# Kernel tuning notes

Measured on AMD Instinct MI355X. Metric: run time of the kernel, lower is better.

## Reference

```python
import jax, jax.numpy as jnp
import numpy as np

S, B, D = 4096, 4, 1024
APERTURE = 256
SCALE = 1.0 / np.sqrt(D)
EPS = 1e-6
NEG_INF = -jnp.inf


def _xavier(key, shape, gain=np.sqrt(2.0)):
    fan_in, fan_out = shape[1], shape[0]
    a = gain * np.sqrt(6.0 / (fan_in + fan_out))
    return jax.random.uniform(key, shape, jnp.float32, -a, a)


def setup_inputs() -> dict:
    key = jax.random.key(0)
    ks = jax.random.split(key, 8)
    return {
        "x": jax.random.normal(ks[0], (S, B, D), jnp.float32),
        "Wk": _xavier(ks[1], (D, D)),
        "Wq": _xavier(ks[2], (D, D)),
        "Wv": _xavier(ks[3], (D, D)),
        "Wp": _xavier(ks[4], (D, D)),
        "W1": _xavier(ks[5], (D, D)),
        "b1": jnp.full((D,), 0.1, jnp.float32),
        "W2": _xavier(ks[6], (1, D)),
        "b2": jnp.full((1,), 0.1, jnp.float32),
        "gamma": jnp.ones((D,), jnp.float32),
        "beta": jnp.zeros((D,), jnp.float32),
    }


def _layer_norm(y, gamma, beta):
    m = jnp.mean(y, axis=-1, keepdims=True)
    v = jnp.mean((y - m) ** 2, axis=-1, keepdims=True)
    return (y - m) * jax.lax.rsqrt(v + EPS) * gamma + beta


def reference(x, Wk, Wq, Wv, Wp, W1, b1, W2, b2, gamma, beta):
    # x: (S, B, D) -> (B, S, D)
    xb = jnp.transpose(x, (1, 0, 2))
    K = jnp.einsum('bsd,ed->bse', xb, Wk)
    Q = jnp.einsum('bsd,ed->bse', xb, Wq)
    V = jnp.einsum('bsd,ed->bse', xb, Wv)
    e = jnp.einsum('bqd,bkd->bqk', Q, K) * SCALE  # (B, S, S)
    # ignore_self: -inf on diagonal
    eye = jnp.eye(S, dtype=bool)
    e = jnp.where(eye[None, :, :], NEG_INF, e)
    # aperture mask: torch masks where tril(e,ap)*triu(e,-ap) == 0
    scope = jnp.tril(e, APERTURE) * jnp.triu(e, -APERTURE)
    e = jnp.where(scope == 0, NEG_INF, e)
    alpha = jax.nn.softmax(e, axis=2)  # dropout is identity at eval
    c = jnp.einsum('bqk,bkd->bqd', alpha, V)
    c = jnp.einsum('bqd,ed->bqe', c, Wp)
    y = c + xb
    y = _layer_norm(y, gamma, beta)
    y = jax.nn.relu(jnp.einsum('bsd,ed->bse', y, W1) + b1)
    y = _layer_norm(y, gamma, beta)
    y = jax.nn.sigmoid(jnp.einsum('bsd,ed->bse', y, W2) + b2)  # (B, S, 1)
    return jnp.transpose(y, (1, 0, 2))  # (S, B, 1)
```

## Files before the change

### kernel.cpp

```cpp
#include <hip/hip_runtime.h>
#include <stdint.h>
#include <math.h>

#define S_LEN 4096
#define BATCH 4
#define DIM   1024
#define AP    256
#define NBLK  32
#define BANDC 640
#define SCALE 0.03125f

typedef __attribute__((ext_vector_type(4))) float f32x4;
typedef __attribute__((ext_vector_type(8))) short bf16x8;

__device__ __forceinline__ ushort f2bf(float f) {
  union { float f; uint32_t u; } v; v.f = f;
  uint32_t r = v.u + 0x7FFFu + ((v.u >> 16) & 1u);
  return (ushort)(r >> 16);
}

__device__ __forceinline__ void gload16(const void* g, void* l) {
  __builtin_amdgcn_global_load_lds((const __attribute__((address_space(1))) void*)g,
                                   (__attribute__((address_space(3))) void*)l,
                                   16, 0, 0);
}

__device__ __forceinline__ float block_sum(float v, float* red) {
  #pragma unroll
  for (int o = 32; o > 0; o >>= 1) v += __shfl_xor(v, o, 64);
  const int w = threadIdx.x >> 6;
  if ((threadIdx.x & 63) == 0) red[w] = v;
  __syncthreads();
  v = red[0] + red[1] + red[2] + red[3];
  __syncthreads();
  return v;
}

__device__ __forceinline__ float block_max(float v, float* red) {
  #pragma unroll
  for (int o = 32; o > 0; o >>= 1) v = fmaxf(v, __shfl_xor(v, o, 64));
  const int w = threadIdx.x >> 6;
  if ((threadIdx.x & 63) == 0) red[w] = v;
  __syncthreads();
  v = fmaxf(fmaxf(red[0], red[1]), fmaxf(red[2], red[3]));
  __syncthreads();
  return v;
}

#define STAGE2(dstbase, g0, g1, kcol) \
  gload16((g0) + (kcol), lds + (dstbase) + stOff); \
  gload16((g1) + (kcol), lds + (dstbase) + 4096 + stOff);

#define MFMA_QUAD(arow, bvec) \
  _Pragma("unroll") for (int m = 0; m < 4; ++m) \
  _Pragma("unroll") for (int n = 0; n < 4; ++n) \
    acc[(arow) + m][n] = __builtin_amdgcn_mfma_f32_16x16x32_bf16(a[m], bvec[n], acc[(arow) + m][n], 0, 0, 0);

#define PHASE_TAIL() \
  __builtin_amdgcn_s_barrier(); \
  asm volatile("s_waitcnt lgkmcnt(0)" ::: "memory"); \
  __builtin_amdgcn_s_setprio(1);

#define PHASE_END() \
  __builtin_amdgcn_s_setprio(0); \
  __builtin_amdgcn_s_barrier();

__device__ __forceinline__ void gemm256_core(
    const ushort* __restrict__ Ablk, int lda,
    const ushort* __restrict__ Bblk, int ldb,
    int K, ushort* __restrict__ lds,
    f32x4 acc[8][4])
{
  const int tid  = threadIdx.x;
  const int lane = tid & 63;
  const int wave = tid >> 6;
  const int wr = wave >> 2;
  const int wn = wave & 3;

  const int srow = tid >> 2;
  const int gseg = (tid & 3) ^ ((tid >> 3) & 3);
  const ushort* gA0 = Ablk + (size_t)srow * lda + gseg * 8;
  const ushort* gA1 = Ablk + (size_t)(srow + 128) * lda + gseg * 8;
  const ushort* gB0 = Bblk + (size_t)srow * ldb + gseg * 8;
  const ushort* gB1 = Bblk + (size_t)(srow + 128) * ldb + gseg * 8;
  const int stOff = wave * 512;

  const int l15 = lane & 15;
  const int seg = (lane >> 4) ^ ((lane >> 1) & 3);
  const int raBase = (wr * 128 + l15) * 32 + seg * 8;
  const int rbBase = (wn * 64  + l15) * 32 + seg * 8;

  const int NT = K >> 6;

  STAGE2(0,     gA0, gA1, 0)
  STAGE2(16384, gB0, gB1, 0)
  STAGE2(8192,  gA0, gA1, 32)
  STAGE2(24576, gB0, gB1, 32)
  asm volatile("s_waitcnt vmcnt(4)" ::: "memory");
  __builtin_amdgcn_s_barrier();

  for (int t = 0; t < NT; ++t) {
    const int rb = (t & 1) * 32768;
    const int sb = ((t + 1) & 1) * 32768;
    const int k1 = (t + 1) << 6;
    const bool more = (t + 1 < NT);

    bf16x8 a[4], b0[4], b1[4];

    #pragma unroll
    for (int m = 0; m < 4; ++m) a[m] = *(const bf16x8*)(lds + rb + raBase + m * 512);
    #pragma unroll
    for (int n = 0; n < 4; ++n) b0[n] = *(const bf16x8*)(lds + rb + 16384 + rbBase + n * 512);
    if (more) { STAGE2(sb, gA0, gA1, k1) }
    PHASE_TAIL()
    MFMA_QUAD(0, b0)
    PHASE_END()

    #pragma unroll
    for (int m = 0; m < 4; ++m) a[m] = *(const bf16x8*)(lds + rb + raBase + (m + 4) * 512);
    if (more) {
      STAGE2(sb + 16384, gB0, gB1, k1)
      asm volatile("s_waitcnt vmcnt(4)" ::: "memory");
    } else {
      asm volatile("s_waitcnt vmcnt(0)" ::: "memory");
    }
    PHASE_TAIL()
    MFMA_QUAD(4, b0)
    PHASE_END()

    #pragma unroll
    for (int m = 0; m < 4; ++m) a[m] = *(const bf16x8*)(lds + rb + 8192 + raBase + m * 512);
    #pragma unroll
    for (int n = 0; n < 4; ++n) b1[n] = *(const bf16x8*)(lds + rb + 24576 + rbBase + n * 512);
    if (more) { STAGE2(sb + 8192, gA0, gA1, k1 + 32) }
    PHASE_TAIL()
    MFMA_QUAD(0, b1)
    PHASE_END()

    #pragma unroll
    for (int m = 0; m < 4; ++m) a[m] = *(const bf16x8*)(lds + rb + 8192 + raBase + (m + 4) * 512);
    if (more) {
      STAGE2(sb + 24576, gB0, gB1, k1 + 32)
      asm volatile("s_waitcnt vmcnt(4)" ::: "memory");
    }
    PHASE_TAIL()
    MFMA_QUAD(4, b1)
    PHASE_END()
  }
}

#define ACC256_ZERO(acc) \
  _Pragma("unroll") for (int m_ = 0; m_ < 8; m_++) \
  _Pragma("unroll") for (int n_ = 0; n_ < 4; n_++) \
  _Pragma("unroll") for (int r_ = 0; r_ < 4; r_++) acc[m_][n_][r_] = 0.0f;

__device__ __forceinline__ void epi256_store_bf16(
    f32x4 acc[8][4], ushort* __restrict__ lds,
    ushort* __restrict__ dst, int rowbase, int colb)
{
  __syncthreads();
  const int lane_ = threadIdx.x & 63;
  const int wave_ = threadIdx.x >> 6;
  const int wrb_ = (wave_ >> 2) * 128;
  const int wnb_ = (wave_ & 3) * 64;
  const int rb_ = (lane_ >> 4) << 2;
  const int cb_ = lane_ & 15;
  #pragma unroll
  for (int m = 0; m < 8; m++)
    #pragma unroll
    for (int n = 0; n < 4; n++)
      #pragma unroll
      for (int r = 0; r < 4; r++) {
        const int rl = wrb_ + m * 16 + rb_ + r;
        const int cl = wnb_ + n * 16 + cb_;
        const int cs = cl ^ (((rl >> 2) & 3) << 4);
        lds[rl * 256 + cs] = f2bf(acc[m][n][r]);
      }
  __syncthreads();
  #pragma unroll
  for (int it = 0; it < 16; ++it) {
    const int chunk = it * 512 + threadIdx.x;
    const int rl = chunk >> 5;
    const int c16 = chunk & 31;
    const int csw = (c16 * 16) ^ (((rl >> 2) & 3) << 5);
    bf16x8 v = *(const bf16x8*)((const char*)lds + rl * 512 + csw);
    *(bf16x8*)(dst + (size_t)(rowbase + rl) * DIM + colb + c16 * 8) = v;
  }
}

#define EPI256_BEGIN(acc) { \
  const int lane_ = threadIdx.x & 63; \
  const int wave_ = threadIdx.x >> 6; \
  const int wrb_ = (wave_ >> 2) * 128; \
  const int wnb_ = (wave_ & 3) * 64; \
  const int rb_ = (lane_ >> 4) << 2; \
  const int cb_ = lane_ & 15; \
  _Pragma("unroll") for (int m_ = 0; m_ < 8; m_++) \
  _Pragma("unroll") for (int n_ = 0; n_ < 4; n_++) \
  _Pragma("unroll") for (int r_ = 0; r_ < 4; r_++) { \
    const int rloc = wrb_ + m_ * 16 + rb_ + r_; \
    const int cloc = wnb_ + n_ * 16 + cb_; \
    const float aval = acc[m_][n_][r_];
#define EPI256_END() } }

__device__ __forceinline__ void gemm_core(
    const ushort* __restrict__ Ablk, int lda,
    const ushort* __restrict__ Bblk, int ldb,
    int k_begin, int k_end,
    ushort* __restrict__ lds,
    f32x4 acc[4][4])
{
  const int tid  = threadIdx.x;
  const int lane = tid & 63;
  const int wr = ((tid >> 7) & 1) * 64;
  const int wc = ((tid >> 6) & 1) * 64;
  const int lr = lane & 15;
  const int seg = (lane >> 4) ^ ((lane >> 1) & 3);

  const int srow = tid >> 2;
  const int gseg = (tid & 3) ^ ((tid >> 3) & 3);
  const ushort* gA0 = Ablk + (size_t)srow * lda + gseg * 8;
  const ushort* gA1 = Ablk + (size_t)(srow + 64) * lda + gseg * 8;
  const ushort* gB0 = Bblk + (size_t)srow * ldb + gseg * 8;
  const ushort* gB1 = Bblk + (size_t)(srow + 64) * ldb + gseg * 8;
  const int stA = (tid >> 6) * 512;

  const int NT = (k_end - k_begin) >> 5;

  gload16(gA0 + k_begin, lds + stA);
  gload16(gA1 + k_begin, lds + 2048 + stA);
  gload16(gB0 + k_begin, lds + 4096 + stA);
  gload16(gB1 + k_begin, lds + 6144 + stA);

  for (int t = 0; t < NT; ++t) {
    if (t + 1 < NT) {
      ushort* buf = lds + ((t + 1) & 1) * 8192;
      const int k0 = k_begin + (t + 1) * 32;
      gload16(gA0 + k0, buf + stA);
      gload16(gA1 + k0, buf + 2048 + stA);
      gload16(gB0 + k0, buf + 4096 + stA);
      gload16(gB1 + k0, buf + 6144 + stA);
      asm volatile("s_waitcnt vmcnt(4)" ::: "memory");
    } else {
      asm volatile("s_waitcnt vmcnt(0)" ::: "memory");
    }
    __builtin_amdgcn_s_barrier();

    const ushort* buf = lds + (t & 1) * 8192;
    bf16x8 af[4], bfv[4];
    #pragma unroll
    for (int m = 0; m < 4; m++)
      af[m] = *(const bf16x8*)(buf + (wr + m * 16 + lr) * 32 + seg * 8);
    #pragma unroll
    for (int n = 0; n < 4; n++)
      bfv[n] = *(const bf16x8*)(buf + 4096 + (wc + n * 16 + lr) * 32 + seg * 8);

    __builtin_amdgcn_s_setprio(1);
    #pragma unroll
    for (int m = 0; m < 4; m++)
      #pragma unroll
      for (int n = 0; n < 4; n++)
        acc[m][n] = __builtin_amdgcn_mfma_f32_16x16x32_bf16(af[m], bfv[n], acc[m][n], 0, 0, 0);
    __builtin_amdgcn_s_setprio(0);
    asm volatile("s_waitcnt lgkmcnt(0)" ::: "memory");
  }
}

#define ACC_ZERO(acc) \
  _Pragma("unroll") for (int m_ = 0; m_ < 4; m_++) \
  _Pragma("unroll") for (int n_ = 0; n_ < 4; n_++) \
  _Pragma("unroll") for (int r_ = 0; r_ < 4; r_++) acc[m_][n_][r_] = 0.0f;

#define EPI_BEGIN(acc) { \
  const int lane_ = threadIdx.x & 63; \
  const int wr_ = ((threadIdx.x >> 7) & 1) * 64; \
  const int wc_ = ((threadIdx.x >> 6) & 1) * 64; \
  const int rb_ = (lane_ >> 4) << 2; \
  const int cb_ = lane_ & 15; \
  _Pragma("unroll") for (int m_ = 0; m_ < 4; m_++) \
  _Pragma("unroll") for (int n_ = 0; n_ < 4; n_++) \
  _Pragma("unroll") for (int r_ = 0; r_ < 4; r_++) { \
    const int rloc = wr_ + m_ * 16 + rb_ + r_; \
    const int cloc = wc_ + n_ * 16 + cb_; \
    const float aval = acc[m_][n_][r_];
#define EPI_END() } }

__global__ __launch_bounds__(256) void prep_x(const float* __restrict__ x, ushort* __restrict__ xb) {
  size_t idx = ((size_t)blockIdx.x * 256 + threadIdx.x) * 4;
  int d = (int)(idx & 1023);
  int s = (int)((idx >> 10) & 4095);
  int b = (int)(idx >> 22);
  float4 v = *(const float4*)(x + ((size_t)s * BATCH + b) * DIM + d);
  ushort4 o;
  o.x = f2bf(v.x); o.y = f2bf(v.y); o.z = f2bf(v.z); o.w = f2bf(v.w);
  *(ushort4*)(xb + idx) = o;
}

__global__ __launch_bounds__(256) void f2bf_all(
    const float* __restrict__ Wk, const float* __restrict__ Wq, const float* __restrict__ Wv,
    const float* __restrict__ Wp, const float* __restrict__ W1,
    ushort* __restrict__ wqkv, ushort* __restrict__ wpb, ushort* __restrict__ w1b)
{
  const int g = blockIdx.x;
  const int which = g >> 10;
  const int idx = ((g & 1023) * 256 + threadIdx.x) * 4;
  const float* src = (which == 0) ? Wk : (which == 1) ? Wq : (which == 2) ? Wv
                   : (which == 3) ? Wp : W1;
  ushort* dst = (which == 0) ? wqkv : (which == 1) ? wqkv + 1048576
              : (which == 2) ? wqkv + 2097152 : (which == 3) ? wpb : w1b;
  float4 v = *(const float4*)(src + idx);
  ushort4 o;
  o.x = f2bf(v.x); o.y = f2bf(v.y); o.z = f2bf(v.z); o.w = f2bf(v.w);
  *(ushort4*)(dst + idx) = o;
}

__global__ __launch_bounds__(512, 2) void qkv_gemm256(
    const ushort* __restrict__ xb, const ushort* __restrict__ wqkv,
    ushort* __restrict__ Kp, ushort* __restrict__ Qp, ushort* __restrict__ Vp)
{
  __shared__ ushort lds[65536];
  const int nid = (blockIdx.x & 7) * 96 + (blockIdx.x >> 3);
  const int by = nid / 12;
  const int bx = nid % 12;
  f32x4 acc[8][4];
  ACC256_ZERO(acc)
  gemm256_core(xb + (size_t)by * 256 * DIM, DIM,
               wqkv + (size_t)bx * 256 * DIM, DIM, DIM, lds, acc);
  ushort* dst = (bx < 4) ? Kp : (bx < 8) ? Qp : Vp;
  epi256_store_bf16(acc, lds, dst, by * 256, (bx & 3) * 256);
}

__global__ __launch_bounds__(512, 2) void wp_gemm256(
    const ushort* __restrict__ cbuf, const ushort* __restrict__ wpb,
    const float* __restrict__ x, float* __restrict__ y0)
{
  __shared__ ushort lds[65536];
  const int nid = (blockIdx.x & 7) * 32 + (blockIdx.x >> 3);
  const int by = nid >> 2;
  const int bx = nid & 3;
  f32x4 acc[8][4];
  ACC256_ZERO(acc)
  gemm256_core(cbuf + (size_t)by * 256 * DIM, DIM,
               wpb + (size_t)bx * 256 * DIM, DIM, DIM, lds, acc);
  EPI256_BEGIN(acc)
    int row = by * 256 + rloc;
    int col = bx * 256 + cloc;
    int b = row >> 12, s = row & 4095;
    y0[(size_t)row * DIM + col] = aval + x[((size_t)s * BATCH + b) * DIM + col];
  EPI256_END()
}

__global__ __launch_bounds__(512, 2) void ffn1_gemm256(
    const ushort* __restrict__ y1, const ushort* __restrict__ w1b,
    const float* __restrict__ b1, float* __restrict__ h0)
{
  __shared__ ushort lds[65536];
  const int nid = (blockIdx.x & 7) * 32 + (blockIdx.x >> 3);
  const int by = nid >> 2;
  const int bx = nid & 3;
  f32x4 acc[8][4];
  ACC256_ZERO(acc)
  gemm256_core(y1 + (size_t)by * 256 * DIM, DIM,
               w1b + (size_t)bx * 256 * DIM, DIM, DIM, lds, acc);
  EPI256_BEGIN(acc)
    int row = by * 256 + rloc;
    int col = bx * 256 + cloc;
    h0[(size_t)row * DIM + col] = fmaxf(aval + b1[col], 0.0f);
  EPI256_END()
}

__global__ __launch_bounds__(256) void transpose_v(const ushort* __restrict__ V, ushort* __restrict__ VT) {
  __shared__ ushort tile[64][66];
  const int s0 = blockIdx.x * 64, d0 = blockIdx.y * 64, b = blockIdx.z;
  const ushort* Vb = V + (size_t)b * S_LEN * DIM;
  ushort* VTb = VT + (size_t)b * DIM * S_LEN;
  #pragma unroll
  for (int it = 0; it < 16; it++) {
    int flat = it * 256 + threadIdx.x;
    int r = flat >> 6, c = flat & 63;
    tile[r][c] = Vb[(size_t)(s0 + r) * DIM + d0 + c];
  }
  __syncthreads();
  #pragma unroll
  for (int it = 0; it < 16; it++) {
    int flat = it * 256 + threadIdx.x;
    int r = flat >> 6, c = flat & 63;
    VTb[(size_t)(d0 + r) * S_LEN + s0 + c] = tile[c][r];
  }
}

__global__ __launch_bounds__(256) void scores_gemm(
    const ushort* __restrict__ Qp, const ushort* __restrict__ Kp,
    float* __restrict__ eband)
{
  const int nid = (blockIdx.x & 7) * 80 + (blockIdx.x >> 3);
  const int b   = nid / 160;
  const int rem = nid % 160;
  const int i   = rem / 5;
  const int jj  = rem % 5;
  const int j   = i - 2 + jj;
  if (j < 0 || j >= NBLK) return;
  __shared__ ushort lds[16384];
  f32x4 acc[4][4];
  ACC_ZERO(acc)
  gemm_core(Qp + ((size_t)b * S_LEN + i * 128) * DIM, DIM,
            Kp + ((size_t)b * S_LEN + j * 128) * DIM, DIM, 0, DIM, lds, acc);
  EPI_BEGIN(acc)
    int q = i * 128 + rloc;
    int k = j * 128 + cloc;
    float v = aval * SCALE;
    int dqk = q - k;
    if (dqk == 0 || dqk > AP || dqk < -AP) v = -INFINITY;
    eband[((size_t)b * S_LEN + q) * BANDC + jj * 128 + cloc] = v;
  EPI_END()
}

__global__ __launch_bounds__(256) void softmax_band(const float* __restrict__ eband,
                                                    ushort* __restrict__ aband)
{
  __shared__ float red[4];
  const int qg = blockIdx.x;
  const int s  = qg & 4095;
  const int i  = s >> 7;
  const float* row = eband + (size_t)qg * BANDC;
  ushort* arow = aband + (size_t)qg * BANDC;

  float vals[3];
  bool  valid[3];
  float mx = -INFINITY;
  #pragma unroll
  for (int t = 0; t < 3; t++) {
    int idx = threadIdx.x + t * 256;
    int jj = idx >> 7;
    int j = i - 2 + jj;
    bool ok = (idx < BANDC) && (j >= 0) && (j < NBLK);
    valid[t] = ok;
    float v = ok ? row[idx] : -INFINITY;
    vals[t] = v;
    mx = fmaxf(mx, v);
  }
  float bmax = block_max(mx, red);
  float ss = 0.0f;
  #pragma unroll
  for (int t = 0; t < 3; t++) {
    float e = valid[t] ? __expf(vals[t] - bmax) : 0.0f;
    vals[t] = e;
    ss += e;
  }
  float inv = 1.0f / block_sum(ss, red);
  #pragma unroll
  for (int t = 0; t < 3; t++) {
    int idx = threadIdx.x + t * 256;
    if (idx < BANDC) arow[idx] = f2bf(vals[t] * inv);
  }
}

__global__ __launch_bounds__(256) void av_gemm(
    const ushort* __restrict__ aband, const ushort* __restrict__ VT,
    ushort* __restrict__ cbuf)
{
  const int nid = (blockIdx.x & 7) * 128 + (blockIdx.x >> 3);
  const int by = nid >> 3;
  const int b = by >> 5, i = by & 31;
  const int bx = nid & 7;
  const int jj_lo = (i < 2) ? (2 - i) : 0;
  const int jj_hi = (i > 29) ? (34 - i) : 5;
  __shared__ ushort lds[16384];
  f32x4 acc[4][4];
  ACC_ZERO(acc)
  const ushort* Ablk = aband + ((size_t)b * S_LEN + i * 128) * BANDC;
  const ushort* Bblk = VT + (size_t)b * DIM * S_LEN + (size_t)bx * 128 * S_LEN + (i - 2) * 128;
  gemm_core(Ablk, BANDC, Bblk, S_LEN, jj_lo * 128, jj_hi * 128, lds, acc);

  __syncthreads();
  {
    const int lane_ = threadIdx.x & 63;
    const int wr_ = ((threadIdx.x >> 7) & 1) * 64;
    const int wc_ = ((threadIdx.x >> 6) & 1) * 64;
    const int rb_ = (lane_ >> 4) << 2;
    const int cb_ = lane_ & 15;
    #pragma unroll
    for (int m = 0; m < 4; m++)
      #pragma unroll
      for (int n = 0; n < 4; n++)
        #pragma unroll
        for (int r = 0; r < 4; r++) {
          const int rl = wr_ + m * 16 + rb_ + r;
          const int cl = wc_ + n * 16 + cb_;
          const int cs = cl ^ (((rl >> 2) & 3) << 4);
          lds[rl * 128 + cs] = f2bf(acc[m][n][r]);
        }
  }
  __syncthreads();
  ushort* dst = cbuf + ((size_t)b * S_LEN + i * 128) * DIM + bx * 128;
  #pragma unroll
  for (int it = 0; it < 8; ++it) {
    const int chunk = it * 256 + threadIdx.x;
    const int rl = chunk >> 4;
    const int c16 = chunk & 15;
    const int csw = (c16 * 16) ^ (((rl >> 2) & 3) << 5);
    bf16x8 v = *(const bf16x8*)((const char*)lds + rl * 256 + csw);
    *(bf16x8*)(dst + (size_t)rl * DIM + c16 * 8) = v;
  }
}

__global__ __launch_bounds__(256) void ln_kernel(const float* __restrict__ y0, ushort* __restrict__ y1,
                                                 const float* __restrict__ gamma, const float* __restrict__ beta)
{
  __shared__ float red[4];
  const size_t q = blockIdx.x;
  const float* row = y0 + q * DIM;
  float v[4];
  #pragma unroll
  for (int t = 0; t < 4; t++) v[t] = row[threadIdx.x + t * 256];
  float mean = block_sum(v[0] + v[1] + v[2] + v[3], red) * (1.0f / DIM);
  float q2 = 0.0f;
  #pragma unroll
  for (int t = 0; t < 4; t++) { float d = v[t] - mean; q2 += d * d; }
  float var = block_sum(q2, red) * (1.0f / DIM);
  float rstd = rsqrtf(var + 1e-6f);
  #pragma unroll
  for (int t = 0; t < 4; t++) {
    int d = threadIdx.x + t * 256;
    y1[q * DIM + d] = f2bf((v[t] - mean) * rstd * gamma[d] + beta[d]);
  }
}

__global__ __launch_bounds__(256) void head_kernel(const float* __restrict__ h0,
    const float* __restrict__ gamma, const float* __restrict__ beta,
    const float* __restrict__ W2, const float* __restrict__ b2,
    float* __restrict__ out)
{
  __shared__ float red[4];
  const int qg = blockIdx.x;
  const int b = qg >> 12, s = qg & 4095;
  const float* row = h0 + (size_t)qg * DIM;
  float v[4];
  #pragma unroll
  for (int t = 0; t < 4; t++) v[t] = row[threadIdx.x + t * 256];
  float mean = block_sum(v[0] + v[1] + v[2] + v[3], red) * (1.0f / DIM);
  float q2 = 0.0f;
  #pragma unroll
  for (int t = 0; t < 4; t++) { float d = v[t] - mean; q2 += d * d; }
  float var = block_sum(q2, red) * (1.0f / DIM);
  float rstd = rsqrtf(var + 1e-6f);
  float part = 0.0f;
  #pragma unroll
  for (int t = 0; t < 4; t++) {
    int d = threadIdx.x + t * 256;
    part += ((v[t] - mean) * rstd * gamma[d] + beta[d]) * W2[d];
  }
  float logit = block_sum(part, red) + b2[0];
  if (threadIdx.x == 0) out[(size_t)s * BATCH + b] = 1.0f / (1.0f + expf(-logit));
}

extern "C" void kernel_launch(void* const* d_in, const int* in_sizes, int n_in,
                              void* d_out, int out_size, void* d_ws, size_t ws_size,
                              hipStream_t stream) {
  const float* x     = (const float*)d_in[0];
  const float* Wk    = (const float*)d_in[1];
  const float* Wq    = (const float*)d_in[2];
  const float* Wv    = (const float*)d_in[3];
  const float* Wp    = (const float*)d_in[4];
  const float* W1    = (const float*)d_in[5];
  const float* b1    = (const float*)d_in[6];
  const float* W2    = (const float*)d_in[7];
  const float* b2    = (const float*)d_in[8];
  const float* gamma = (const float*)d_in[9];
  const float* beta  = (const float*)d_in[10];
  float* out = (float*)d_out;

  char* w = (char*)d_ws;
  ushort* xb   = (ushort*)(w + 0);
  ushort* wqkv = (ushort*)(w + 33554432);
  ushort* wpb  = (ushort*)(w + 39845888);
  ushort* w1b  = (ushort*)(w + 41943040);
  ushort* Qp   = (ushort*)(w + 44040192);
  ushort* Kp   = (ushort*)(w + 77594624);
  ushort* Vp   = (ushort*)(w + 111149056);
  ushort* VT   = (ushort*)(w + 144703488);
  float*  big  = (float*)(w + 178257920);
  ushort* aband = Qp;
  ushort* cbuf  = Kp;
  ushort* y1    = Vp;
  float* eband = big;
  float* y0    = big;
  float* h0    = big;

  prep_x<<<16384, 256, 0, stream>>>(x, xb);
  f2bf_all<<<5120, 256, 0, stream>>>(Wk, Wq, Wv, Wp, W1, wqkv, wpb, w1b);

  qkv_gemm256<<<768, 512, 0, stream>>>(xb, wqkv, Kp, Qp, Vp);
  transpose_v<<<dim3(64, 16, 4), 256, 0, stream>>>(Vp, VT);
  scores_gemm<<<640, 256, 0, stream>>>(Qp, Kp, eband);
  softmax_band<<<16384, 256, 0, stream>>>(eband, aband);
  av_gemm<<<1024, 256, 0, stream>>>(aband, VT, cbuf);
  wp_gemm256<<<256, 512, 0, stream>>>(cbuf, wpb, x, y0);
  ln_kernel<<<16384, 256, 0, stream>>>(y0, y1, gamma, beta);
  ffn1_gemm256<<<256, 512, 0, stream>>>(y1, w1b, b1, h0);
  head_kernel<<<16384, 256, 0, stream>>>(h0, gamma, beta, W2, b2, out);
}
```

Measured before the change: 377.5 us.

## Replace four-phase barrier-synchronized GEMM loop with one barrier per K tile

Restructures the GEMM main loop. The per-phase barrier pairs and partial vmcnt waits are dropped. Fragments go into separate register sets so LDS reads and global prefetches can be issued ahead of the MFMA groups, with a single vmcnt(0) wait and barrier at the end of each K iteration. The aim is to cut barrier overhead and let MFMA overlap loads, at the cost of more registers and a full drain of outstanding loads every iteration.

After: 376.2 us. No clear change (-0.3%).

```diff
diff --git a/kernel.cpp b/kernel.cpp
--- a/kernel.cpp
+++ b/kernel.cpp
@@ -51,19 +51,12 @@
   gload16((g0) + (kcol), lds + (dstbase) + stOff); \
   gload16((g1) + (kcol), lds + (dstbase) + 4096 + stOff);
 
-#define MFMA_QUAD(arow, bvec) \
+#define MFMA_QUAD(arow, av, bv) \
+  __builtin_amdgcn_s_setprio(1); \
   _Pragma("unroll") for (int m = 0; m < 4; ++m) \
   _Pragma("unroll") for (int n = 0; n < 4; ++n) \
-    acc[(arow) + m][n] = __builtin_amdgcn_mfma_f32_16x16x32_bf16(a[m], bvec[n], acc[(arow) + m][n], 0, 0, 0);
-
-#define PHASE_TAIL() \
-  __builtin_amdgcn_s_barrier(); \
-  asm volatile("s_waitcnt lgkmcnt(0)" ::: "memory"); \
-  __builtin_amdgcn_s_setprio(1);
-
-#define PHASE_END() \
-  __builtin_amdgcn_s_setprio(0); \
-  __builtin_amdgcn_s_barrier();
+    acc[(arow) + m][n] = __builtin_amdgcn_mfma_f32_16x16x32_bf16(av[m], bv[n], acc[(arow) + m][n], 0, 0, 0); \
+  __builtin_amdgcn_s_setprio(0);
 
 __device__ __forceinline__ void gemm256_core(
     const ushort* __restrict__ Ablk, int lda,
@@ -96,7 +89,7 @@
   STAGE2(16384, gB0, gB1, 0)
   STAGE2(8192,  gA0, gA1, 32)
   STAGE2(24576, gB0, gB1, 32)
-  asm volatile("s_waitcnt vmcnt(4)" ::: "memory");
+  asm volatile("s_waitcnt vmcnt(0)" ::: "memory");
   __builtin_amdgcn_s_barrier();
 
   for (int t = 0; t < NT; ++t) {
@@ -105,47 +98,41 @@
     const int k1 = (t + 1) << 6;
     const bool more = (t + 1 < NT);
 
-    bf16x8 a[4], b0[4], b1[4];
-
-    #pragma unroll
-    for (int m = 0; m < 4; ++m) a[m] = *(const bf16x8*)(lds + rb + raBase + m * 512);
-    #pragma unroll
-    for (int n = 0; n < 4; ++n) b0[n] = *(const bf16x8*)(lds + rb + 16384 + rbBase + n * 512);
-    if (more) { STAGE2(sb, gA0, gA1, k1) }
-    PHASE_TAIL()
-    MFMA_QUAD(0, b0)
-    PHASE_END()
-
-    #pragma unroll
-    for (int m = 0; m < 4; ++m) a[m] = *(const bf16x8*)(lds + rb + raBase + (m + 4) * 512);
+    bf16x8 aA[4], aB[4], bA[4], bB[4];
+
+    #pragma unroll
+    for (int m = 0; m < 4; ++m) aA[m] = *(const bf16x8*)(lds + rb + raBase + m * 512);
+    #pragma unroll
+    for (int n = 0; n < 4; ++n) bA[n] = *(const bf16x8*)(lds + rb + 16384 + rbBase + n * 512);
+    #pragma unroll
+    for (int m = 0; m < 4; ++m) aB[m] = *(const bf16x8*)(lds + rb + raBase + (m + 4) * 512);
     if (more) {
+      STAGE2(sb,         gA0, gA1, k1)
       STAGE2(sb + 16384, gB0, gB1, k1)
-      asm volatile("s_waitcnt vmcnt(4)" ::: "memory");
-    } else {
-      asm volatile("s_waitcnt vmcnt(0)" ::: "memory");
     }
-    PHASE_TAIL()
-    MFMA_QUAD(4, b0)
-    PHASE_END()
-
-    #pragma unroll
-    for (int m = 0; m < 4; ++m) a[m] = *(const bf16x8*)(lds + rb + 8192 + raBase + m * 512);
-    #pragma unroll
-    for (int n = 0; n < 4; ++n) b1[n] = *(const bf16x8*)(lds + rb + 24576 + rbBase + n * 512);
-    if (more) { STAGE2(sb + 8192, gA0, gA1, k1 + 32) }
-    PHASE_TAIL()
-    MFMA_QUAD(0, b1)
-    PHASE_END()
-
-    #pragma unroll
-    for (int m = 0; m < 4; ++m) a[m] = *(const bf16x8*)(lds + rb + 8192 + raBase + (m + 4) * 512);
+
+    MFMA_QUAD(0, aA, bA)
+
+    #pragma unroll
+    for (int m = 0; m < 4; ++m) aA[m] = *(const bf16x8*)(lds + rb + 8192 + raBase + m * 512);
+    #pragma unroll
+    for (int n = 0; n < 4; ++n) bB[n] = *(const bf16x8*)(lds + rb + 24576 + rbBase + n * 512);
     if (more) {
+      STAGE2(sb + 8192,  gA0, gA1, k1 + 32)
       STAGE2(sb + 24576, gB0, gB1, k1 + 32)
-      asm volatile("s_waitcnt vmcnt(4)" ::: "memory");
     }
-    PHASE_TAIL()
-    MFMA_QUAD(4, b1)
-    PHASE_END()
+
+    MFMA_QUAD(4, aB, bA)
+
+    #pragma unroll
+    for (int m = 0; m < 4; ++m) aB[m] = *(const bf16x8*)(lds + rb + 8192 + raBase + (m + 4) * 512);
+
+    MFMA_QUAD(0, aA, bB)
+
+    MFMA_QUAD(4, aB, bB)
+
+    asm volatile("s_waitcnt vmcnt(0)" ::: "memory");
+    __builtin_amdgcn_s_barrier();
   }
 }
 
```
